# Kernel tuning notes

Hardware: AMD Instinct MI355X
Metric: run time of the kernel (lower is better)

## Reference

```python
import jax, jax.numpy as jnp
import numpy as np

D = 768
HEAD_SIZE = 64  # D / num_heads = 768 / 12

def setup_inputs() -> dict:
    key = jax.random.key(0)
    k1, k2, k3, k4 = jax.random.split(key, 4)
    ix = jax.random.normal(k1, (8, 4096, D), dtype=jnp.float32)
    # Linear(D, head_size, bias=False) weights; stored as [D, head_size] for x @ W
    scale = 1.0 / np.sqrt(D)
    Wk = jax.random.uniform(k2, (D, HEAD_SIZE), dtype=jnp.float32, minval=-scale, maxval=scale)
    Wq = jax.random.uniform(k3, (D, HEAD_SIZE), dtype=jnp.float32, minval=-scale, maxval=scale)
    Wv = jax.random.uniform(k4, (D, HEAD_SIZE), dtype=jnp.float32, minval=-scale, maxval=scale)
    return {"ix": ix, "Wk": Wk, "Wq": Wq, "Wv": Wv}

def reference(ix, Wk, Wq, Wv):
    # ix: [B, S, D]
    k = ix @ Wk  # [B, S, H]
    q = ix @ Wq  # [B, S, H]
    v = ix @ Wv  # [B, S, H]
    scale = 1.0 / jnp.sqrt(jnp.asarray(HEAD_SIZE, ix.dtype))
    wei = jnp.einsum('bsh,bth->bst', q, k) * scale  # [B, S, S]
    wei = jax.nn.softmax(wei, axis=-1)
    out = jnp.einsum('bst,bth->bsh', wei, v)  # [B, S, H]
    return out
```

## Files before the change

kernel.cpp:

```cpp
#include <hip/hip_runtime.h>
#include <hip/hip_bf16.h>

#define D_DIM 768
#define HS 64
#define SEQ 4096
#define NBATCH 8

typedef short bf8 __attribute__((ext_vector_type(8)));
typedef float f4 __attribute__((ext_vector_type(4)));

static __device__ __forceinline__ short f2b(float x) {
    __hip_bfloat16 h = __float2bfloat16(x);
    return __builtin_bit_cast(short, h);
}
static __device__ __forceinline__ short f2b_rh(float x) {
    unsigned u = __builtin_bit_cast(unsigned, x);
    return (short)((u + 0x8000u) >> 16);
}

#if defined(__has_builtin)
#if __has_builtin(__builtin_amdgcn_exp2f)
#define EXP2F(x) __builtin_amdgcn_exp2f(x)
#endif
#endif
#ifndef EXP2F
#define EXP2F(x) exp2f(x)
#endif

__global__ __launch_bounds__(256) void wconv_kernel(
    const float* __restrict__ Wk, const float* __restrict__ Wq,
    const float* __restrict__ Wv, short* __restrict__ wt)
{
    int tid = blockIdx.x * 256 + threadIdx.x;
    int mat = tid / (D_DIM * HS);
    int rem = tid - mat * (D_DIM * HS);
    int k = rem >> 6;
    int n = rem & 63;
    const float* W = (mat == 0) ? Wk : (mat == 1) ? Wq : Wv;
    float scale = (mat == 1) ? 0.18033688011112042f : 1.0f;
    wt[(mat * HS + n) * D_DIM + k] = f2b(W[rem] * scale);
}

__global__ __launch_bounds__(256) void proj_kernel(
    const float* __restrict__ ix, const short* __restrict__ wt,
    short* __restrict__ qg, short* __restrict__ kg, short* __restrict__ vg)
{
    __shared__ short ixl[2][64 * 40];
    __shared__ short wtl[2][192 * 40];

    const int t = threadIdx.x;
    const int wave = t >> 6, lane = t & 63;
    const int m = lane & 15, quad = lane >> 4;
    const int wy = wave >> 1, wx = wave & 1;
    const int m0 = blockIdx.x * 64;

    const int srow = t >> 2;
    const int skoff = (t & 3) * 8;

    f4 xr0, xr1;
    bf8 wr0, wr1, wr2, wr3;

    auto load_chunk = [&](int c) {
        const float* px = ix + (m0 + srow) * D_DIM + c * 32 + skoff;
        xr0 = *(const f4*)px;
        xr1 = *(const f4*)(px + 4);
        if (t < 192) {
            const short* pw = wt + t * D_DIM + c * 32;
            wr0 = *(const bf8*)(pw);
            wr1 = *(const bf8*)(pw + 8);
            wr2 = *(const bf8*)(pw + 16);
            wr3 = *(const bf8*)(pw + 24);
        }
    };
    auto write_chunk = [&](int p) {
        bf8 xw;
        #pragma unroll
        for (int i = 0; i < 4; ++i) { xw[i] = f2b(xr0[i]); xw[i + 4] = f2b(xr1[i]); }
        *(bf8*)(&ixl[p][srow * 40 + skoff]) = xw;
        if (t < 192) {
            *(bf8*)(&wtl[p][t * 40 + 0])  = wr0;
            *(bf8*)(&wtl[p][t * 40 + 8])  = wr1;
            *(bf8*)(&wtl[p][t * 40 + 16]) = wr2;
            *(bf8*)(&wtl[p][t * 40 + 24]) = wr3;
        }
    };

    f4 acc[2][6] = {};

    load_chunk(0); write_chunk(0); __syncthreads();

    for (int c = 0; c < 24; ++c) {
        const int p = c & 1;
        if (c + 1 < 24) load_chunk(c + 1);

        bf8 a0 = *(const bf8*)(&ixl[p][(wy * 32 + m) * 40 + quad * 8]);
        bf8 a1 = *(const bf8*)(&ixl[p][(wy * 32 + 16 + m) * 40 + quad * 8]);
        bf8 bb[6];
        #pragma unroll
        for (int nt = 0; nt < 6; ++nt)
            bb[nt] = *(const bf8*)(&wtl[p][(wx * 96 + nt * 16 + m) * 40 + quad * 8]);
        #pragma unroll
        for (int nt = 0; nt < 6; ++nt) {
            acc[0][nt] = __builtin_amdgcn_mfma_f32_16x16x32_bf16(a0, bb[nt], acc[0][nt], 0, 0, 0);
            acc[1][nt] = __builtin_amdgcn_mfma_f32_16x16x32_bf16(a1, bb[nt], acc[1][nt], 0, 0, 0);
        }

        if (c + 1 < 24) { write_chunk((c + 1) & 1); __syncthreads(); }
    }

    #pragma unroll
    for (int mt = 0; mt < 2; ++mt) {
        const int row = m0 + wy * 32 + mt * 16 + quad * 4;
        #pragma unroll
        for (int nt = 0; nt < 6; ++nt) {
            const int cb = wx * 96 + nt * 16;
            short* op = (cb < 64) ? kg : (cb < 128) ? qg : vg;
            const int n = (cb & 63) + m;
            #pragma unroll
            for (int r = 0; r < 4; ++r)
                op[(row + r) * HS + n] = f2b(acc[mt][nt][r]);
        }
    }
}

__global__ __launch_bounds__(256) void attn_kernel(
    const short* __restrict__ qg, const short* __restrict__ kg,
    const short* __restrict__ vg, float* __restrict__ num0,
    float* __restrict__ num1, float* __restrict__ den0,
    float* __restrict__ den1)
{
    __shared__ short kl[2][64 * 72];
    __shared__ short vl[2][64 * 70];

    const int t = threadIdx.x;
    const int wave = t >> 6, lane = t & 63;
    const int m = lane & 15, quad = lane >> 4;

    const int flat = blockIdx.x;
    const int lg = (flat & 7) * 64 + (flat >> 3);
    const int qx = lg & 31;
    const int yz = lg >> 5;
    const int ks = yz & 1;
    const int b  = yz >> 1;

    const int rbase = b * SEQ;
    const int kbase = rbase + ks * (SEQ / 2);
    const int qw = qx * 128 + wave * 32;

    float* __restrict__ nump = ks == 0 ? num0 : num1;
    float* __restrict__ denp = ks == 0 ? den0 : den1;

    bf8 qf[2][2];
    #pragma unroll
    for (int nq = 0; nq < 2; ++nq)
        #pragma unroll
        for (int st = 0; st < 2; ++st)
            qf[nq][st] = *(const bf8*)(qg + (rbase + qw + nq * 16 + m) * HS + st * 32 + quad * 8);

    const int srow = t >> 2, soff = (t & 3) * 16;
    const int jp = t >> 3, dg = t & 7;
    const int j0 = jp * 2;

    uint4 kr0, kr1, vr0, vr1;
    auto load_chunk = [&](int c) {
        const short* pk = kg + (kbase + c * 64 + srow) * HS + soff;
        kr0 = *(const uint4*)pk; kr1 = *(const uint4*)(pk + 8);
        const short* pv = vg + (kbase + c * 64 + j0) * HS + dg * 8;
        vr0 = *(const uint4*)pv; vr1 = *(const uint4*)(pv + HS);
    };
    auto write_chunk = [&](int p) {
        *(bf8*)(&kl[p][srow * 72 + soff])     = __builtin_bit_cast(bf8, kr0);
        *(bf8*)(&kl[p][srow * 72 + soff + 8]) = __builtin_bit_cast(bf8, kr1);
        bf8 v0 = __builtin_bit_cast(bf8, vr0), v1 = __builtin_bit_cast(bf8, vr1);
        #pragma unroll
        for (int i = 0; i < 8; ++i) {
            const int d = dg * 8 + i;
            unsigned val = (unsigned short)v0[i] | ((unsigned)(unsigned short)v1[i] << 16);
            *(unsigned*)(&vl[p][d * 70 + j0]) = val;
        }
    };

    f4 o[2][4] = {};
    float den[2] = {0.f, 0.f};

    load_chunk(0); write_chunk(0); __syncthreads();

    for (int c = 0; c < SEQ / 128; ++c) {
        const int p = c & 1;
        if (c + 1 < SEQ / 128) load_chunk(c + 1);

        #pragma unroll
        for (int g = 0; g < 2; ++g) {
            bf8 kA0 = *(const bf8*)(&kl[p][(g * 32 + m) * 72 + quad * 8]);
            bf8 kA1 = *(const bf8*)(&kl[p][(g * 32 + m) * 72 + 32 + quad * 8]);
            bf8 kB0 = *(const bf8*)(&kl[p][(g * 32 + 16 + m) * 72 + quad * 8]);
            bf8 kB1 = *(const bf8*)(&kl[p][(g * 32 + 16 + m) * 72 + 32 + quad * 8]);

            bf8 vf[4];
            #pragma unroll
            for (int dt = 0; dt < 4; ++dt) {
                const short* vp = &vl[p][(dt * 16 + m) * 70 + g * 32 + quad * 4];
                unsigned a0 = *(const unsigned*)vp;
                unsigned a1 = *(const unsigned*)(vp + 2);
                unsigned b0 = *(const unsigned*)(vp + 16);
                unsigned b1 = *(const unsigned*)(vp + 18);
                uint4 u; u.x = a0; u.y = a1; u.z = b0; u.w = b1;
                vf[dt] = __builtin_bit_cast(bf8, u);
            }

            #pragma unroll
            for (int nq = 0; nq < 2; ++nq) {
                f4 sa = {0.f, 0.f, 0.f, 0.f}, sb = {0.f, 0.f, 0.f, 0.f};
                sa = __builtin_amdgcn_mfma_f32_16x16x32_bf16(kA0, qf[nq][0], sa, 0, 0, 0);
                sa = __builtin_amdgcn_mfma_f32_16x16x32_bf16(kA1, qf[nq][1], sa, 0, 0, 0);
                sb = __builtin_amdgcn_mfma_f32_16x16x32_bf16(kB0, qf[nq][0], sb, 0, 0, 0);
                sb = __builtin_amdgcn_mfma_f32_16x16x32_bf16(kB1, qf[nq][1], sb, 0, 0, 0);
                float e0 = EXP2F(sa[0]), e1 = EXP2F(sa[1]), e2 = EXP2F(sa[2]), e3 = EXP2F(sa[3]);
                float e4 = EXP2F(sb[0]), e5 = EXP2F(sb[1]), e6 = EXP2F(sb[2]), e7 = EXP2F(sb[3]);
                den[nq] += ((e0 + e1) + (e2 + e3)) + ((e4 + e5) + (e6 + e7));
                bf8 pf;
                pf[0] = f2b_rh(e0); pf[1] = f2b_rh(e1); pf[2] = f2b_rh(e2); pf[3] = f2b_rh(e3);
                pf[4] = f2b_rh(e4); pf[5] = f2b_rh(e5); pf[6] = f2b_rh(e6); pf[7] = f2b_rh(e7);
                #pragma unroll
                for (int dt = 0; dt < 4; ++dt)
                    o[nq][dt] = __builtin_amdgcn_mfma_f32_16x16x32_bf16(vf[dt], pf, o[nq][dt], 0, 0, 0);
            }
        }

        if (c + 1 < SEQ / 128) { write_chunk((c + 1) & 1); __syncthreads(); }
    }

    #pragma unroll
    for (int nq = 0; nq < 2; ++nq) {
        float d = den[nq];
        d += __shfl_xor(d, 16, 64);
        d += __shfl_xor(d, 32, 64);
        const int orow = rbase + qw + nq * 16 + m;
        if (quad == 0) denp[orow] = d;
        #pragma unroll
        for (int dt = 0; dt < 4; ++dt)
            *(f4*)(nump + orow * HS + dt * 16 + quad * 4) = o[nq][dt];
    }
}

__global__ __launch_bounds__(256) void reduce_kernel(
    float* __restrict__ out, const float* __restrict__ num1,
    const float* __restrict__ den0, const float* __restrict__ den1)
{
    const int gid = blockIdx.x * 256 + threadIdx.x;
    const int base = gid * 4;
    const int r = base >> 6;
    f4 n0 = *(const f4*)(out + base);
    f4 n1 = *(const f4*)(num1 + base);
    const float rs = 1.0f / (den0[r] + den1[r]);
    f4 res;
    #pragma unroll
    for (int i = 0; i < 4; ++i) res[i] = (n0[i] + n1[i]) * rs;
    *(f4*)(out + base) = res;
}

extern "C" void kernel_launch(void* const* d_in, const int* in_sizes, int n_in,
                              void* d_out, int out_size, void* d_ws, size_t ws_size,
                              hipStream_t stream) {
    const float* ix = (const float*)d_in[0];
    const float* Wk = (const float*)d_in[1];
    const float* Wq = (const float*)d_in[2];
    const float* Wv = (const float*)d_in[3];
    float* out = (float*)d_out;

    const size_t NQKV = (size_t)NBATCH * SEQ * HS;
    short* qg = (short*)d_ws;
    short* kg = qg + NQKV;
    short* vg = kg + NQKV;
    short* wt = vg + NQKV;
    char*  fbase = (char*)(wt + 3 * D_DIM * HS);
    float* num1 = (float*)fbase;
    float* den0 = num1 + NQKV;
    float* den1 = den0 + (size_t)NBATCH * SEQ;

    wconv_kernel<<<(3 * D_DIM * HS) / 256, 256, 0, stream>>>(Wk, Wq, Wv, wt);
    proj_kernel<<<(NBATCH * SEQ) / 64, 256, 0, stream>>>(ix, wt, qg, kg, vg);
    attn_kernel<<<512, 256, 0, stream>>>(qg, kg, vg, out, num1, den0, den1);
    reduce_kernel<<<(int)(NQKV / (256 * 4)), 256, 0, stream>>>(out, num1, den0, den1);
}
```

Before: 228.2 us.

## Split attention keys four ways, swizzle V LDS layout, shrink projection tiles

The attention kernel now splits the key range into four parts instead of two, launching 1024 blocks with a min-blocks-per-CU launch bound so more of the GPU is occupied. The reduce kernel sums four partial numerators and denominators. V is stored in LDS with an XOR-swizzled layout so each MFMA operand becomes a single 16-byte LDS read instead of four 4-byte reads. bf16 packing of probabilities uses a perm instruction. The projection kernel uses 32-row tiles to double its block count. In exchange, the extra partials add global memory traffic for the intermediate buffers and the reduce step.

```diff
diff --git a/kernel.cpp b/kernel.cpp
--- a/kernel.cpp
+++ b/kernel.cpp
@@ -7,15 +7,17 @@
 #define NBATCH 8
 
 typedef short bf8 __attribute__((ext_vector_type(8)));
+typedef short bf4 __attribute__((ext_vector_type(4)));
 typedef float f4 __attribute__((ext_vector_type(4)));
 
 static __device__ __forceinline__ short f2b(float x) {
     __hip_bfloat16 h = __float2bfloat16(x);
     return __builtin_bit_cast(short, h);
 }
-static __device__ __forceinline__ short f2b_rh(float x) {
-    unsigned u = __builtin_bit_cast(unsigned, x);
-    return (short)((u + 0x8000u) >> 16);
+static __device__ __forceinline__ unsigned pk2(float x, float y) {
+    unsigned ux = __builtin_bit_cast(unsigned, x) + 0x8000u;
+    unsigned uy = __builtin_bit_cast(unsigned, y) + 0x8000u;
+    return __builtin_amdgcn_perm(uy, ux, 0x07060302u);
 }
 
 #if defined(__has_builtin)
@@ -45,25 +47,23 @@
     const float* __restrict__ ix, const short* __restrict__ wt,
     short* __restrict__ qg, short* __restrict__ kg, short* __restrict__ vg)
 {
-    __shared__ short ixl[2][64 * 40];
+    __shared__ short ixl[2][32 * 40];
     __shared__ short wtl[2][192 * 40];
 
     const int t = threadIdx.x;
     const int wave = t >> 6, lane = t & 63;
     const int m = lane & 15, quad = lane >> 4;
-    const int wy = wave >> 1, wx = wave & 1;
-    const int m0 = blockIdx.x * 64;
-
-    const int srow = t >> 2;
-    const int skoff = (t & 3) * 8;
-
-    f4 xr0, xr1;
+    const int m0 = blockIdx.x * 32;
+
+    const int srow = t >> 3;
+    const int skoff = (t & 7) * 4;
+
+    f4 xr;
     bf8 wr0, wr1, wr2, wr3;
 
     auto load_chunk = [&](int c) {
         const float* px = ix + (m0 + srow) * D_DIM + c * 32 + skoff;
-        xr0 = *(const f4*)px;
-        xr1 = *(const f4*)(px + 4);
+        xr = *(const f4*)px;
         if (t < 192) {
             const short* pw = wt + t * D_DIM + c * 32;
             wr0 = *(const bf8*)(pw);
@@ -73,10 +73,10 @@
         }
     };
     auto write_chunk = [&](int p) {
-        bf8 xw;
-        #pragma unroll
-        for (int i = 0; i < 4; ++i) { xw[i] = f2b(xr0[i]); xw[i + 4] = f2b(xr1[i]); }
-        *(bf8*)(&ixl[p][srow * 40 + skoff]) = xw;
+        bf4 xw;
+        #pragma unroll
+        for (int i = 0; i < 4; ++i) xw[i] = f2b(xr[i]);
+        *(bf4*)(&ixl[p][srow * 40 + skoff]) = xw;
         if (t < 192) {
             *(bf8*)(&wtl[p][t * 40 + 0])  = wr0;
             *(bf8*)(&wtl[p][t * 40 + 8])  = wr1;
@@ -85,7 +85,7 @@
         }
     };
 
-    f4 acc[2][6] = {};
+    f4 acc[2][3] = {};
 
     load_chunk(0); write_chunk(0); __syncthreads();
 
@@ -93,14 +93,14 @@
         const int p = c & 1;
         if (c + 1 < 24) load_chunk(c + 1);
 
-        bf8 a0 = *(const bf8*)(&ixl[p][(wy * 32 + m) * 40 + quad * 8]);
-        bf8 a1 = *(const bf8*)(&ixl[p][(wy * 32 + 16 + m) * 40 + quad * 8]);
-        bf8 bb[6];
-        #pragma unroll
-        for (int nt = 0; nt < 6; ++nt)
-            bb[nt] = *(const bf8*)(&wtl[p][(wx * 96 + nt * 16 + m) * 40 + quad * 8]);
-        #pragma unroll
-        for (int nt = 0; nt < 6; ++nt) {
+        bf8 a0 = *(const bf8*)(&ixl[p][(m) * 40 + quad * 8]);
+        bf8 a1 = *(const bf8*)(&ixl[p][(16 + m) * 40 + quad * 8]);
+        bf8 bb[3];
+        #pragma unroll
+        for (int nt = 0; nt < 3; ++nt)
+            bb[nt] = *(const bf8*)(&wtl[p][(wave * 48 + nt * 16 + m) * 40 + quad * 8]);
+        #pragma unroll
+        for (int nt = 0; nt < 3; ++nt) {
             acc[0][nt] = __builtin_amdgcn_mfma_f32_16x16x32_bf16(a0, bb[nt], acc[0][nt], 0, 0, 0);
             acc[1][nt] = __builtin_amdgcn_mfma_f32_16x16x32_bf16(a1, bb[nt], acc[1][nt], 0, 0, 0);
         }
@@ -110,10 +110,10 @@
 
     #pragma unroll
     for (int mt = 0; mt < 2; ++mt) {
-        const int row = m0 + wy * 32 + mt * 16 + quad * 4;
-        #pragma unroll
-        for (int nt = 0; nt < 6; ++nt) {
-            const int cb = wx * 96 + nt * 16;
+        const int row = m0 + mt * 16 + quad * 4;
+        #pragma unroll
+        for (int nt = 0; nt < 3; ++nt) {
+            const int cb = wave * 48 + nt * 16;
             short* op = (cb < 64) ? kg : (cb < 128) ? qg : vg;
             const int n = (cb & 63) + m;
             #pragma unroll
@@ -123,32 +123,33 @@
     }
 }
 
-__global__ __launch_bounds__(256) void attn_kernel(
+__global__ __launch_bounds__(256, 4) void attn_kernel(
     const short* __restrict__ qg, const short* __restrict__ kg,
     const short* __restrict__ vg, float* __restrict__ num0,
-    float* __restrict__ num1, float* __restrict__ den0,
-    float* __restrict__ den1)
+    float* __restrict__ num1, float* __restrict__ num2,
+    float* __restrict__ num3, float* __restrict__ den0,
+    float* __restrict__ den1, float* __restrict__ den2,
+    float* __restrict__ den3)
 {
     __shared__ short kl[2][64 * 72];
-    __shared__ short vl[2][64 * 70];
+    __shared__ short vl[2][64 * 64];
 
     const int t = threadIdx.x;
     const int wave = t >> 6, lane = t & 63;
     const int m = lane & 15, quad = lane >> 4;
 
     const int flat = blockIdx.x;
-    const int lg = (flat & 7) * 64 + (flat >> 3);
+    const int lg = (flat & 7) * 128 + (flat >> 3);
     const int qx = lg & 31;
-    const int yz = lg >> 5;
-    const int ks = yz & 1;
-    const int b  = yz >> 1;
+    const int ks = (lg >> 5) & 3;
+    const int b  = lg >> 7;
 
     const int rbase = b * SEQ;
-    const int kbase = rbase + ks * (SEQ / 2);
+    const int kbase = rbase + ks * (SEQ / 4);
     const int qw = qx * 128 + wave * 32;
 
-    float* __restrict__ nump = ks == 0 ? num0 : num1;
-    float* __restrict__ denp = ks == 0 ? den0 : den1;
+    float* __restrict__ nump = (ks == 0) ? num0 : (ks == 1) ? num1 : (ks == 2) ? num2 : num3;
+    float* __restrict__ denp = (ks == 0) ? den0 : (ks == 1) ? den1 : (ks == 2) ? den2 : den3;
 
     bf8 qf[2][2];
     #pragma unroll
@@ -160,6 +161,13 @@
     const int srow = t >> 2, soff = (t & 3) * 16;
     const int jp = t >> 3, dg = t & 7;
     const int j0 = jp * 2;
+    const int jj = j0 & 31;
+    const int gj = j0 >> 5;
+    const int vq = (jj >> 2) & 3;
+    const int vh = (jj >> 4) & 1;
+    const int vb = (jj & 3) >> 1;
+    const int vcol_base = vh * 4 + 2 * vb;
+    const int vchunk_l = 4 * gj + vq;
 
     uint4 kr0, kr1, vr0, vr1;
     auto load_chunk = [&](int c) {
@@ -175,8 +183,9 @@
         #pragma unroll
         for (int i = 0; i < 8; ++i) {
             const int d = dg * 8 + i;
+            const int chunk = vchunk_l ^ (i ^ dg);
             unsigned val = (unsigned short)v0[i] | ((unsigned)(unsigned short)v1[i] << 16);
-            *(unsigned*)(&vl[p][d * 70 + j0]) = val;
+            *(unsigned*)(&vl[p][d * 64 + chunk * 8 + vcol_base]) = val;
         }
     };
 
@@ -185,9 +194,10 @@
 
     load_chunk(0); write_chunk(0); __syncthreads();
 
-    for (int c = 0; c < SEQ / 128; ++c) {
+    const int NCH = SEQ / 4 / 64;
+    for (int c = 0; c < NCH; ++c) {
         const int p = c & 1;
-        if (c + 1 < SEQ / 128) load_chunk(c + 1);
+        if (c + 1 < NCH) load_chunk(c + 1);
 
         #pragma unroll
         for (int g = 0; g < 2; ++g) {
@@ -199,13 +209,10 @@
             bf8 vf[4];
             #pragma unroll
             for (int dt = 0; dt < 4; ++dt) {
-                const short* vp = &vl[p][(dt * 16 + m) * 70 + g * 32 + quad * 4];
-                unsigned a0 = *(const unsigned*)vp;
-                unsigned a1 = *(const unsigned*)(vp + 2);
-                unsigned b0 = *(const unsigned*)(vp + 16);
-                unsigned b1 = *(const unsigned*)(vp + 18);
-                uint4 u; u.x = a0; u.y = a1; u.z = b0; u.w = b1;
-                vf[dt] = __builtin_bit_cast(bf8, u);
+                const int row = dt * 16 + m;
+                const int key = (m & 7) ^ (2 * dt + (m >> 3));
+                const int chunk = (g * 4 + quad) ^ key;
+                vf[dt] = *(const bf8*)(&vl[p][row * 64 + chunk * 8]);
             }
 
             #pragma unroll
@@ -218,16 +225,17 @@
                 float e0 = EXP2F(sa[0]), e1 = EXP2F(sa[1]), e2 = EXP2F(sa[2]), e3 = EXP2F(sa[3]);
                 float e4 = EXP2F(sb[0]), e5 = EXP2F(sb[1]), e6 = EXP2F(sb[2]), e7 = EXP2F(sb[3]);
                 den[nq] += ((e0 + e1) + (e2 + e3)) + ((e4 + e5) + (e6 + e7));
-                bf8 pf;
-                pf[0] = f2b_rh(e0); pf[1] = f2b_rh(e1); pf[2] = f2b_rh(e2); pf[3] = f2b_rh(e3);
-                pf[4] = f2b_rh(e4); pf[5] = f2b_rh(e5); pf[6] = f2b_rh(e6); pf[7] = f2b_rh(e7);
+                uint4 pu;
+                pu.x = pk2(e0, e1); pu.y = pk2(e2, e3);
+                pu.z = pk2(e4, e5); pu.w = pk2(e6, e7);
+                bf8 pf = __builtin_bit_cast(bf8, pu);
                 #pragma unroll
                 for (int dt = 0; dt < 4; ++dt)
                     o[nq][dt] = __builtin_amdgcn_mfma_f32_16x16x32_bf16(vf[dt], pf, o[nq][dt], 0, 0, 0);
             }
         }
 
-        if (c + 1 < SEQ / 128) { write_chunk((c + 1) & 1); __syncthreads(); }
+        if (c + 1 < NCH) { write_chunk((c + 1) & 1); __syncthreads(); }
     }
 
     #pragma unroll
@@ -245,17 +253,21 @@
 
 __global__ __launch_bounds__(256) void reduce_kernel(
     float* __restrict__ out, const float* __restrict__ num1,
-    const float* __restrict__ den0, const float* __restrict__ den1)
+    const float* __restrict__ num2, const float* __restrict__ num3,
+    const float* __restrict__ den0, const float* __restrict__ den1,
+    const float* __restrict__ den2, const float* __restrict__ den3)
 {
     const int gid = blockIdx.x * 256 + threadIdx.x;
     const int base = gid * 4;
     const int r = base >> 6;
     f4 n0 = *(const f4*)(out + base);
     f4 n1 = *(const f4*)(num1 + base);
-    const float rs = 1.0f / (den0[r] + den1[r]);
+    f4 n2 = *(const f4*)(num2 + base);
+    f4 n3 = *(const f4*)(num3 + base);
+    const float rs = 1.0f / ((den0[r] + den1[r]) + (den2[r] + den3[r]));
     f4 res;
     #pragma unroll
-    for (int i = 0; i < 4; ++i) res[i] = (n0[i] + n1[i]) * rs;
+    for (int i = 0; i < 4; ++i) res[i] = ((n0[i] + n1[i]) + (n2[i] + n3[i])) * rs;
     *(f4*)(out + base) = res;
 }
 
@@ -275,11 +287,17 @@
     short* wt = vg + NQKV;
     char*  fbase = (char*)(wt + 3 * D_DIM * HS);
     float* num1 = (float*)fbase;
-    float* den0 = num1 + NQKV;
+    float* num2 = num1 + NQKV;
+    float* num3 = num2 + NQKV;
+    float* den0 = num3 + NQKV;
     float* den1 = den0 + (size_t)NBATCH * SEQ;
+    float* den2 = den1 + (size_t)NBATCH * SEQ;
+    float* den3 = den2 + (size_t)NBATCH * SEQ;
 
     wconv_kernel<<<(3 * D_DIM * HS) / 256, 256, 0, stream>>>(Wk, Wq, Wv, wt);
-    proj_kernel<<<(NBATCH * SEQ) / 64, 256, 0, stream>>>(ix, wt, qg, kg, vg);
-    attn_kernel<<<512, 256, 0, stream>>>(qg, kg, vg, out, num1, den0, den1);
-    reduce_kernel<<<(int)(NQKV / (256 * 4)), 256, 0, stream>>>(out, num1, den0, den1);
-}
+    proj_kernel<<<(NBATCH * SEQ) / 32, 256, 0, stream>>>(ix, wt, qg, kg, vg);
+    attn_kernel<<<1024, 256, 0, stream>>>(qg, kg, vg, out, num1, num2, num3,
+                                          den0, den1, den2, den3);
+    reduce_kernel<<<(int)(NQKV / (256 * 4)), 256, 0, stream>>>(
+        out, num1, num2, num3, den0, den1, den2, den3);
+}
```

New measurement: 249.4 us. +9.3%, slower.
